# Performance work log

Hardware: AMD Instinct MI355X
Metric: run time of the kernel (lower is better)

Reference implementation:

```python
import jax, jax.numpy as jnp
import numpy as np
import math

P = 7          # patch / kernel size (must be odd for onion-peeling: N = 1+4*m*(m+1) = P*P)
EPS = 1e-6
EPS_W = 0.5

def _ball_dirs():
    u = [np.array([[1.0, 0.0]])]
    s = [np.zeros(1)]
    for k in range(1, P // 2 + 1):
        n = 8 * k
        th = np.linspace(0.0, 2.0 * math.pi * (1.0 - 1.0 / n), n)
        u.append(np.stack([np.cos(th), np.sin(th)], 1))
        s.append(np.full(n, k / (P // 2)))
    return (np.concatenate(u, 0).astype(np.float32), np.concatenate(s).astype(np.float32))

_U, _S = _ball_dirs()  # [N,2], [N], N == P*P == 49

def _forward(x, metric_w, metric_b, proj_w, proj_b):
    B, C, H, W = x.shape
    Hp, Wp = H // P, W // P
    u = jnp.asarray(_U)
    s = jnp.asarray(_S)
    # metric net: strided conv -> 7 params per patch
    params = jax.lax.conv_general_dilated(
        x, metric_w, (P, P), 'VALID',
        dimension_numbers=('NCHW', 'OIHW', 'NCHW')) + metric_b[None, :, None, None]
    v_raw = jnp.moveaxis(params[:, :2], 1, -1)                      # [B,Hp,Wp,2]
    v = v_raw / jnp.maximum(jnp.linalg.norm(v_raw, axis=-1, keepdims=True), 1e-12)
    eig = 2.0 * jax.nn.sigmoid(jnp.moveaxis(params[:, 2:4], 1, -1))  # [B,Hp,Wp,2]
    scale = 0.5 + 1.5 * jax.nn.sigmoid(jnp.moveaxis(params[:, 4:5], 1, -1))
    eig = eig * scale
    vp = jnp.stack([-v[..., 1], v[..., 0]], -1)
    R = jnp.stack([v, vp], -1)                                      # [B,Hp,Wp,2,2] (columns v, v_perp)
    M = R @ (eig[..., None] * jnp.swapaxes(R, -1, -2))              # R diag(eig) R^T
    w = params[:, 5:7]                                              # [B,2,Hp,Wp]
    w = w * (1.0 - EPS_W) * jax.nn.sigmoid(jnp.linalg.norm(w, axis=1, keepdims=True))
    # Finsler-Randers norm F(u) = sqrt(u^T M u + eps) + w.u for all N unit dirs
    quad = jnp.einsum('nj,bhwij,ni->bnhw', u, M, u)                 # [B,N,Hp,Wp]
    drift = jnp.einsum('bihw,ni->bnhw', w, u)
    F_u = jnp.sqrt(quad + EPS) + drift
    y = (u[None, :, :, None, None] / (F_u[:, :, None] + EPS)
         * s[None, :, None, None, None])                            # [B,N,2,Hp,Wp]
    y = y.reshape(B, P, P, 2, Hp, Wp)[:, :, :, ::-1]                # flip last coord pair (x,y)->(y,x)
    gi = jnp.arange(P, dtype=x.dtype) - P // 2
    grid = jnp.stack(jnp.meshgrid(gi, gi, indexing='ij'), -1)       # [P,P,2]
    off = y - grid[None, :, :, :, None, None]                       # [B,P,P,2,Hp,Wp]
    off_y = jnp.transpose(off[:, :, :, 0], (0, 3, 4, 1, 2))         # [B,Hp,Wp,P,P]
    off_x = jnp.transpose(off[:, :, :, 1], (0, 3, 4, 1, 2))
    base_h = (jnp.arange(Hp, dtype=x.dtype) * P)[None, :, None, None, None]
    base_w = (jnp.arange(Wp, dtype=x.dtype) * P)[None, None, :, None, None]
    ki = jnp.arange(P, dtype=x.dtype)
    py = off_y + base_h + ki[None, None, None, :, None]             # sample rows
    px = off_x + base_w + ki[None, None, None, None, :]             # sample cols
    # bilinear sampling with zero padding (torchvision deform_conv2d semantics)
    y0 = jnp.floor(py)
    x0 = jnp.floor(px)
    wy = py - y0
    wx = px - x0

    def gather(yi, xi):
        valid = (yi >= 0) & (yi <= H - 1) & (xi >= 0) & (xi <= W - 1)
        yc = jnp.clip(yi, 0, H - 1).astype(jnp.int32)
        xc = jnp.clip(xi, 0, W - 1).astype(jnp.int32)
        vals = jax.vmap(lambda img, yy, xx: img[:, yy, xx])(x, yc, xc)  # [B,C,Hp,Wp,P,P]
        return vals * valid[:, None].astype(x.dtype)

    sampled = (gather(y0, x0) * ((1 - wy) * (1 - wx))[:, None]
               + gather(y0, x0 + 1) * ((1 - wy) * wx)[:, None]
               + gather(y0 + 1, x0) * (wy * (1 - wx))[:, None]
               + gather(y0 + 1, x0 + 1) * (wy * wx)[:, None])       # [B,C,Hp,Wp,P,P]
    out = jnp.einsum('bchwij,ecij->behw', sampled, proj_w) + proj_b[None, :, None, None]
    return jnp.moveaxis(out.reshape(B, out.shape[1], -1), 1, 2)     # [B, Hp*Wp, E]

def setup_inputs():
    key = jax.random.key(0)
    k0, k1, k2 = jax.random.split(key, 3)
    B, C, H, W, E = 64, 3, 224, 224, 384
    x = jax.random.normal(k0, (B, C, H, W), jnp.float32)
    metric_w = jax.random.normal(k1, (7, C, P, P), jnp.float32) / math.sqrt(C * P * P)
    metric_b = jnp.zeros((7,), jnp.float32)
    proj_w = jax.random.normal(k2, (E, C, P, P), jnp.float32) / (P * math.sqrt(C))
    proj_b = jnp.zeros((E,), jnp.float32)
    return {"x": x, "metric_w": metric_w, "metric_b": metric_b,
            "proj_w": proj_w, "proj_b": proj_b}

def reference(x, metric_w, metric_b, proj_w, proj_b):
    return _forward(x, metric_w, metric_b, proj_w, proj_b)
```

## Files before the change

kernel.cpp:

```cpp
#include <hip/hip_runtime.h>
#include <math.h>

#define PP   7
#define NDIR 49
#define CIN  3
#define KK   147
#define KPAD 160
#define EE   384
#define HH   224
#define WW   224
#define GG   16
#define TB   256
#define SSTR 17
#define NPX  112

typedef __attribute__((ext_vector_type(8))) __bf16 bf16x8;
typedef __attribute__((ext_vector_type(4))) float  f32x4;

__device__ __forceinline__ float sigmoidf_(float v) {
    return 1.0f / (1.0f + expf(-v));
}

__global__ void pack_kernel(const float* __restrict__ x,
                            const float* __restrict__ pw,
                            float* __restrict__ xp,
                            unsigned short* __restrict__ pwB,
                            int npix4) {
    int idx = blockIdx.x * blockDim.x + threadIdx.x;
    if (idx < EE * KPAD) {
        int e = idx / KPAD;
        int k = idx - e * KPAD;
        float v = (k < KK) ? pw[e * KK + k] : 0.0f;
        __bf16 h = (__bf16)v;
        pwB[idx] = *(unsigned short*)&h;
    }
    if (idx < npix4) {
        const int ppi = HH * WW / 4;
        int b = idx / ppi;
        int p = (idx - b * ppi) * 4;
        const float* xb = x + (size_t)b * (CIN * HH * WW) + p;
        f32x4 r0 = *(const f32x4*)(xb);
        f32x4 r1 = *(const f32x4*)(xb + HH * WW);
        f32x4 r2 = *(const f32x4*)(xb + 2 * HH * WW);
        float* op = xp + ((size_t)b * (HH * WW) + p) * 4;
        #pragma unroll
        for (int i = 0; i < 4; ++i) {
            f32x4 v = {r0[i], r1[i], r2[i], 0.0f};
            *(f32x4*)(op + i * 4) = v;
        }
    }
}

template<bool PACKED>
__launch_bounds__(TB, 8)
__global__ void fused_kernel(const float* __restrict__ x,
                             const float* __restrict__ xp,
                             const float* __restrict__ mw,
                             const float* __restrict__ mb,
                             const unsigned short* __restrict__ pwB,
                             const float* __restrict__ pb,
                             float* __restrict__ out) {
    __shared__ float mws[7 * KK];
    __shared__ float dirs[NDIR][3];
    __shared__ float par_s[GG][8];
    __shared__ float der_s[GG][5];
    __shared__ __align__(16) float buf[3136];

    const int t   = threadIdx.x;
    const int blk = blockIdx.x;
    const int b   = blk >> 6;
    const int rem = blk & 63;
    const int hp  = rem >> 1;
    const int wp0 = (rem & 1) * GG;
    const size_t m0 = (size_t)blk * GG;
    const int row0 = hp * PP;
    const int col0 = wp0 * PP;

    for (int i = t; i < 7 * KK; i += TB) mws[i] = mw[i];
    if (t >= 64 && t < 64 + NDIR) {
        int n = t - 64;
        float u0, u1, s;
        if (n == 0)      { u0 = 1.0f; u1 = 0.0f; s = 0.0f; }
        else if (n < 9)  { float th = (float)(n - 1)  * 0.78539816339744831f; u0 = cosf(th); u1 = sinf(th); s = 0.33333334f; }
        else if (n < 25) { float th = (float)(n - 9)  * 0.39269908169872414f; u0 = cosf(th); u1 = sinf(th); s = 0.66666669f; }
        else             { float th = (float)(n - 25) * 0.26179938779914941f; u0 = cosf(th); u1 = sinf(th); s = 1.0f; }
        dirs[n][0] = u0; dirs[n][1] = u1; dirs[n][2] = s;
    }

    if (PACKED) {
        for (int item = t; item < 7 * NPX; item += TB) {
            int i = item / NPX, px = item - i * NPX;
            f32x4 v = *(const f32x4*)(xp + ((size_t)((b * HH + row0 + i) * WW) + col0 + px) * 4);
            *(f32x4*)&buf[item * 4] = v;
        }
    } else {
        for (int item = t; item < CIN * 7 * NPX; item += TB) {
            int c = item / (7 * NPX), r2 = item - c * (7 * NPX);
            int i = r2 / NPX, px = r2 - i * NPX;
            buf[item] = x[(size_t)b * (CIN * HH * WW) + (size_t)c * (HH * WW)
                          + (size_t)(row0 + i) * WW + col0 + px];
        }
    }
    __syncthreads();

    if (t < 112) {
        int prm = t >> 4, g = t & 15;
        float acc = mb[prm];
        const float* wrow = &mws[prm * KK];
        if (PACKED) {
            #pragma unroll 1
            for (int c = 0; c < CIN; ++c) {
                #pragma unroll 1
                for (int i = 0; i < 7; ++i) {
                    const float* bp = &buf[(i * NPX + g * 7) * 4 + c];
                    const float* wr = &wrow[c * 49 + i * 7];
                    #pragma unroll
                    for (int j = 0; j < 7; ++j)
                        acc = fmaf(bp[j * 4], wr[j], acc);
                }
            }
        } else {
            #pragma unroll 1
            for (int c = 0; c < CIN; ++c) {
                #pragma unroll 1
                for (int i = 0; i < 7; ++i) {
                    const float* bp = &buf[(c * 7 + i) * NPX + g * 7];
                    const float* wr = &wrow[c * 49 + i * 7];
                    #pragma unroll
                    for (int j = 0; j < 7; ++j)
                        acc = fmaf(bp[j], wr[j], acc);
                }
            }
        }
        par_s[g][prm] = acc;
    }
    __syncthreads();

    if (t < GG) {
        float a0 = par_s[t][0], a1 = par_s[t][1], a2 = par_s[t][2], a3 = par_s[t][3];
        float a4 = par_s[t][4], a5 = par_s[t][5], a6 = par_s[t][6];
        float nrm = sqrtf(a0 * a0 + a1 * a1);
        float inv = 1.0f / fmaxf(nrm, 1e-12f);
        float v0 = a0 * inv, v1 = a1 * inv;
        float e0 = 2.0f * sigmoidf_(a2);
        float e1 = 2.0f * sigmoidf_(a3);
        float sc = 0.5f + 1.5f * sigmoidf_(a4);
        e0 *= sc; e1 *= sc;
        float wn  = sqrtf(a5 * a5 + a6 * a6);
        float wsc = 0.5f * sigmoidf_(wn);
        der_s[t][0] = e0 * v0 * v0 + e1 * v1 * v1;
        der_s[t][1] = (e0 - e1) * v0 * v1;
        der_s[t][2] = e0 * v1 * v1 + e1 * v0 * v0;
        der_s[t][3] = a5 * wsc;
        der_s[t][4] = a6 * wsc;
    }
    __syncthreads();

    const float* xb = x + (size_t)b * (CIN * HH * WW);
    const size_t pbase = (size_t)b * (HH * WW);
    for (int item = t; item < GG * NDIR; item += TB) {
        int g = item / NDIR;
        int n = item - g * NDIR;
        float u0 = dirs[n][0], u1 = dirs[n][1], s = dirs[n][2];
        float M00 = der_s[g][0], M01 = der_s[g][1], M11 = der_s[g][2];
        float w0 = der_s[g][3], w1 = der_s[g][4];
        float quad  = u0 * u0 * M00 + 2.0f * u0 * u1 * M01 + u1 * u1 * M11;
        float drift = w0 * u0 + w1 * u1;
        float F = sqrtf(quad + 1e-6f) + drift;
        float r = s / (F + 1e-6f);
        float py = (float)(row0 + 3) + u1 * r;
        float px = (float)(col0 + g * PP + 3) + u0 * r;
        float y0f = floorf(py), x0f = floorf(px);
        float y1f = y0f + 1.0f, x1f = x0f + 1.0f;
        float wy = py - y0f, wx = px - x0f;
        bool vy0 = (y0f >= 0.0f) && (y0f <= (float)(HH - 1));
        bool vy1 = (y1f >= 0.0f) && (y1f <= (float)(HH - 1));
        bool vx0 = (x0f >= 0.0f) && (x0f <= (float)(WW - 1));
        bool vx1 = (x1f >= 0.0f) && (x1f <= (float)(WW - 1));
        int iy0 = (int)fminf(fmaxf(y0f, 0.0f), (float)(HH - 1));
        int iy1 = (int)fminf(fmaxf(y1f, 0.0f), (float)(HH - 1));
        int ix0 = (int)fminf(fmaxf(x0f, 0.0f), (float)(WW - 1));
        int ix1 = (int)fminf(fmaxf(x1f, 0.0f), (float)(WW - 1));
        float w00 = (1.0f - wy) * (1.0f - wx);
        float w01 = (1.0f - wy) * wx;
        float w10 = wy * (1.0f - wx);
        float w11 = wy * wx;
        if (PACKED) {
            float c00 = w00 * ((vy0 && vx0) ? 1.0f : 0.0f);
            float c01 = w01 * ((vy0 && vx1) ? 1.0f : 0.0f);
            float c10 = w10 * ((vy1 && vx0) ? 1.0f : 0.0f);
            float c11 = w11 * ((vy1 && vx1) ? 1.0f : 0.0f);
            f32x4 q00 = *(const f32x4*)(xp + (pbase + (size_t)(iy0 * WW + ix0)) * 4);
            f32x4 q01 = *(const f32x4*)(xp + (pbase + (size_t)(iy0 * WW + ix1)) * 4);
            f32x4 q10 = *(const f32x4*)(xp + (pbase + (size_t)(iy1 * WW + ix0)) * 4);
            f32x4 q11 = *(const f32x4*)(xp + (pbase + (size_t)(iy1 * WW + ix1)) * 4);
            #pragma unroll
            for (int c = 0; c < CIN; ++c) {
                buf[(c * NDIR + n) * SSTR + g] =
                    q00[c] * c00 + q01[c] * c01 + q10[c] * c10 + q11[c] * c11;
            }
        } else {
            #pragma unroll
            for (int c = 0; c < CIN; ++c) {
                const float* xc = xb + c * (HH * WW);
                float v00 = (vy0 && vx0) ? xc[iy0 * WW + ix0] : 0.0f;
                float v01 = (vy0 && vx1) ? xc[iy0 * WW + ix1] : 0.0f;
                float v10 = (vy1 && vx0) ? xc[iy1 * WW + ix0] : 0.0f;
                float v11 = (vy1 && vx1) ? xc[iy1 * WW + ix1] : 0.0f;
                buf[(c * NDIR + n) * SSTR + g] =
                    v00 * w00 + v01 * w01 + v10 * w10 + v11 * w11;
            }
        }
    }
    __syncthreads();

    const int lane = t & 63;
    const int wv   = t >> 6;
    const int nrow = lane & 15;
    const int hi   = lane >> 4;

    bf16x8 afr[5];
    #pragma unroll
    for (int ks = 0; ks < 5; ++ks) {
        #pragma unroll
        for (int j = 0; j < 8; ++j) {
            int k = ks * 32 + hi * 8 + j;
            float v = (k < KK) ? buf[k * SSTR + nrow] : 0.0f;
            afr[ks][j] = (__bf16)v;
        }
    }

    #pragma unroll
    for (int q = 0; q < 6; ++q) {
        int tile = wv * 6 + q;
        int e    = tile * 16 + nrow;
        const unsigned short* brow = pwB + (size_t)e * KPAD + hi * 8;
        f32x4 acc = {0.0f, 0.0f, 0.0f, 0.0f};
        #pragma unroll
        for (int ks = 0; ks < 5; ++ks) {
            bf16x8 bfr = *(const bf16x8*)&brow[ks * 32];
            acc = __builtin_amdgcn_mfma_f32_16x16x32_bf16(afr[ks], bfr, acc, 0, 0, 0);
        }
        float bias = pb[e];
        #pragma unroll
        for (int r = 0; r < 4; ++r) {
            out[(m0 + hi * 4 + r) * EE + e] = acc[r] + bias;
        }
    }
}

extern "C" void kernel_launch(void* const* d_in, const int* in_sizes, int n_in,
                              void* d_out, int out_size, void* d_ws, size_t ws_size,
                              hipStream_t stream) {
    const float* x  = (const float*)d_in[0];
    const float* mw = (const float*)d_in[1];
    const float* mb = (const float*)d_in[2];
    const float* pw = (const float*)d_in[3];
    const float* pb = (const float*)d_in[4];
    float* out = (float*)d_out;

    unsigned short* pwB = (unsigned short*)d_ws;
    float* xp = (float*)((char*)d_ws + (size_t)(1 << 17));

    const int B = in_sizes[0] / (CIN * HH * WW);
    const int npix = B * HH * WW;
    const int npix4 = npix / 4;
    const size_t need = (size_t)(1 << 17) + (size_t)npix * 4 * sizeof(float);
    const bool packed = ws_size >= need;

    if (packed) {
        int grid = (npix4 > EE * KPAD ? npix4 : EE * KPAD);
        pack_kernel<<<(grid + 255) / 256, 256, 0, stream>>>(x, pw, xp, pwB, npix4);
        fused_kernel<true><<<B * 64, TB, 0, stream>>>(x, xp, mw, mb, pwB, pb, out);
    } else {
        pack_kernel<<<(EE * KPAD + 255) / 256, 256, 0, stream>>>(x, pw, xp, pwB, 0);
        fused_kernel<false><<<B * 64, TB, 0, stream>>>(x, xp, mw, mb, pwB, pb, out);
    }
}
```

Baseline: 200.1 us.

## Batch bilinear gather loads and transpose MFMA operands for vectorized output stores

Refactors the sampling geometry into a helper and, on the packed path, manually unrolls the gather so two items issue all eight 16-byte loads before any use, with a scheduling barrier to expose memory-level parallelism. Swaps the MFMA operand order so each lane owns four consecutive embedding columns of one token, allowing float4 bias loads and float4 output stores instead of strided scalar stores. Lowers the launch-bounds occupancy hint from 8 to 6 to give the extra in-flight loads register room, at the cost of fewer resident waves.

```diff
diff --git a/kernel.cpp b/kernel.cpp
--- a/kernel.cpp
+++ b/kernel.cpp
@@ -51,8 +51,53 @@
     }
 }
 
+struct GInfo {
+    int g, n;
+    int o00, o01, o10, o11;
+    float c00, c01, c10, c11;
+};
+
+__device__ __forceinline__ GInfo geom_(int item, int row0, int col0,
+                                       const float dirs[NDIR][3],
+                                       const float der[GG][5]) {
+    GInfo r;
+    r.g = item / NDIR;
+    r.n = item - r.g * NDIR;
+    float u0 = dirs[r.n][0], u1 = dirs[r.n][1], s = dirs[r.n][2];
+    float M00 = der[r.g][0], M01 = der[r.g][1], M11 = der[r.g][2];
+    float w0 = der[r.g][3], w1 = der[r.g][4];
+    float quad  = u0 * u0 * M00 + 2.0f * u0 * u1 * M01 + u1 * u1 * M11;
+    float drift = w0 * u0 + w1 * u1;
+    float F = sqrtf(quad + 1e-6f) + drift;
+    float rr = s / (F + 1e-6f);
+    float py = (float)(row0 + 3) + u1 * rr;
+    float px = (float)(col0 + r.g * PP + 3) + u0 * rr;
+    float y0f = floorf(py), x0f = floorf(px);
+    float y1f = y0f + 1.0f, x1f = x0f + 1.0f;
+    float wy = py - y0f, wx = px - x0f;
+    r.c00 = (1.0f - wy) * (1.0f - wx);
+    r.c01 = (1.0f - wy) * wx;
+    r.c10 = wy * (1.0f - wx);
+    r.c11 = wy * wx;
+    bool vy0 = (y0f >= 0.0f) && (y0f <= (float)(HH - 1));
+    bool vy1 = (y1f >= 0.0f) && (y1f <= (float)(HH - 1));
+    bool vx0 = (x0f >= 0.0f) && (x0f <= (float)(WW - 1));
+    bool vx1 = (x1f >= 0.0f) && (x1f <= (float)(WW - 1));
+    r.c00 *= (vy0 && vx0) ? 1.0f : 0.0f;
+    r.c01 *= (vy0 && vx1) ? 1.0f : 0.0f;
+    r.c10 *= (vy1 && vx0) ? 1.0f : 0.0f;
+    r.c11 *= (vy1 && vx1) ? 1.0f : 0.0f;
+    int iy0 = (int)fminf(fmaxf(y0f, 0.0f), (float)(HH - 1));
+    int iy1 = (int)fminf(fmaxf(y1f, 0.0f), (float)(HH - 1));
+    int ix0 = (int)fminf(fmaxf(x0f, 0.0f), (float)(WW - 1));
+    int ix1 = (int)fminf(fmaxf(x1f, 0.0f), (float)(WW - 1));
+    r.o00 = iy0 * WW + ix0; r.o01 = iy0 * WW + ix1;
+    r.o10 = iy1 * WW + ix0; r.o11 = iy1 * WW + ix1;
+    return r;
+}
+
 template<bool PACKED>
-__launch_bounds__(TB, 8)
+__launch_bounds__(TB, 6)
 __global__ void fused_kernel(const float* __restrict__ x,
                              const float* __restrict__ xp,
                              const float* __restrict__ mw,
@@ -87,10 +132,11 @@
         dirs[n][0] = u0; dirs[n][1] = u1; dirs[n][2] = s;
     }
 
+    const size_t pbase = (size_t)b * (HH * WW);
     if (PACKED) {
         for (int item = t; item < 7 * NPX; item += TB) {
             int i = item / NPX, px = item - i * NPX;
-            f32x4 v = *(const f32x4*)(xp + ((size_t)((b * HH + row0 + i) * WW) + col0 + px) * 4);
+            f32x4 v = *(const f32x4*)(xp + (pbase + (size_t)(row0 + i) * WW + col0 + px) * 4);
             *(f32x4*)&buf[item * 4] = v;
         }
     } else {
@@ -156,59 +202,61 @@
     }
     __syncthreads();
 
-    const float* xb = x + (size_t)b * (CIN * HH * WW);
-    const size_t pbase = (size_t)b * (HH * WW);
-    for (int item = t; item < GG * NDIR; item += TB) {
-        int g = item / NDIR;
-        int n = item - g * NDIR;
-        float u0 = dirs[n][0], u1 = dirs[n][1], s = dirs[n][2];
-        float M00 = der_s[g][0], M01 = der_s[g][1], M11 = der_s[g][2];
-        float w0 = der_s[g][3], w1 = der_s[g][4];
-        float quad  = u0 * u0 * M00 + 2.0f * u0 * u1 * M01 + u1 * u1 * M11;
-        float drift = w0 * u0 + w1 * u1;
-        float F = sqrtf(quad + 1e-6f) + drift;
-        float r = s / (F + 1e-6f);
-        float py = (float)(row0 + 3) + u1 * r;
-        float px = (float)(col0 + g * PP + 3) + u0 * r;
-        float y0f = floorf(py), x0f = floorf(px);
-        float y1f = y0f + 1.0f, x1f = x0f + 1.0f;
-        float wy = py - y0f, wx = px - x0f;
-        bool vy0 = (y0f >= 0.0f) && (y0f <= (float)(HH - 1));
-        bool vy1 = (y1f >= 0.0f) && (y1f <= (float)(HH - 1));
-        bool vx0 = (x0f >= 0.0f) && (x0f <= (float)(WW - 1));
-        bool vx1 = (x1f >= 0.0f) && (x1f <= (float)(WW - 1));
-        int iy0 = (int)fminf(fmaxf(y0f, 0.0f), (float)(HH - 1));
-        int iy1 = (int)fminf(fmaxf(y1f, 0.0f), (float)(HH - 1));
-        int ix0 = (int)fminf(fmaxf(x0f, 0.0f), (float)(WW - 1));
-        int ix1 = (int)fminf(fmaxf(x1f, 0.0f), (float)(WW - 1));
-        float w00 = (1.0f - wy) * (1.0f - wx);
-        float w01 = (1.0f - wy) * wx;
-        float w10 = wy * (1.0f - wx);
-        float w11 = wy * wx;
-        if (PACKED) {
-            float c00 = w00 * ((vy0 && vx0) ? 1.0f : 0.0f);
-            float c01 = w01 * ((vy0 && vx1) ? 1.0f : 0.0f);
-            float c10 = w10 * ((vy1 && vx0) ? 1.0f : 0.0f);
-            float c11 = w11 * ((vy1 && vx1) ? 1.0f : 0.0f);
-            f32x4 q00 = *(const f32x4*)(xp + (pbase + (size_t)(iy0 * WW + ix0)) * 4);
-            f32x4 q01 = *(const f32x4*)(xp + (pbase + (size_t)(iy0 * WW + ix1)) * 4);
-            f32x4 q10 = *(const f32x4*)(xp + (pbase + (size_t)(iy1 * WW + ix0)) * 4);
-            f32x4 q11 = *(const f32x4*)(xp + (pbase + (size_t)(iy1 * WW + ix1)) * 4);
-            #pragma unroll
-            for (int c = 0; c < CIN; ++c) {
-                buf[(c * NDIR + n) * SSTR + g] =
-                    q00[c] * c00 + q01[c] * c01 + q10[c] * c10 + q11[c] * c11;
-            }
-        } else {
+    if (PACKED) {
+        const float* base = xp + pbase * 4;
+        {
+            GInfo A = geom_(t,      row0, col0, dirs, der_s);
+            GInfo B = geom_(t + TB, row0, col0, dirs, der_s);
+            f32x4 qa0 = *(const f32x4*)(base + (size_t)A.o00 * 4);
+            f32x4 qa1 = *(const f32x4*)(base + (size_t)A.o01 * 4);
+            f32x4 qa2 = *(const f32x4*)(base + (size_t)A.o10 * 4);
+            f32x4 qa3 = *(const f32x4*)(base + (size_t)A.o11 * 4);
+            f32x4 qb0 = *(const f32x4*)(base + (size_t)B.o00 * 4);
+            f32x4 qb1 = *(const f32x4*)(base + (size_t)B.o01 * 4);
+            f32x4 qb2 = *(const f32x4*)(base + (size_t)B.o10 * 4);
+            f32x4 qb3 = *(const f32x4*)(base + (size_t)B.o11 * 4);
+            __builtin_amdgcn_sched_barrier(0);
+            #pragma unroll
+            for (int c = 0; c < CIN; ++c)
+                buf[(c * NDIR + A.n) * SSTR + A.g] =
+                    qa0[c] * A.c00 + qa1[c] * A.c01 + qa2[c] * A.c10 + qa3[c] * A.c11;
+            #pragma unroll
+            for (int c = 0; c < CIN; ++c)
+                buf[(c * NDIR + B.n) * SSTR + B.g] =
+                    qb0[c] * B.c00 + qb1[c] * B.c01 + qb2[c] * B.c10 + qb3[c] * B.c11;
+        }
+        {
+            GInfo C = geom_(t + 2 * TB, row0, col0, dirs, der_s);
+            f32x4 q0 = *(const f32x4*)(base + (size_t)C.o00 * 4);
+            f32x4 q1 = *(const f32x4*)(base + (size_t)C.o01 * 4);
+            f32x4 q2 = *(const f32x4*)(base + (size_t)C.o10 * 4);
+            f32x4 q3 = *(const f32x4*)(base + (size_t)C.o11 * 4);
+            #pragma unroll
+            for (int c = 0; c < CIN; ++c)
+                buf[(c * NDIR + C.n) * SSTR + C.g] =
+                    q0[c] * C.c00 + q1[c] * C.c01 + q2[c] * C.c10 + q3[c] * C.c11;
+        }
+        if (t < GG * NDIR - 3 * TB) {
+            GInfo D = geom_(t + 3 * TB, row0, col0, dirs, der_s);
+            f32x4 q0 = *(const f32x4*)(base + (size_t)D.o00 * 4);
+            f32x4 q1 = *(const f32x4*)(base + (size_t)D.o01 * 4);
+            f32x4 q2 = *(const f32x4*)(base + (size_t)D.o10 * 4);
+            f32x4 q3 = *(const f32x4*)(base + (size_t)D.o11 * 4);
+            #pragma unroll
+            for (int c = 0; c < CIN; ++c)
+                buf[(c * NDIR + D.n) * SSTR + D.g] =
+                    q0[c] * D.c00 + q1[c] * D.c01 + q2[c] * D.c10 + q3[c] * D.c11;
+        }
+    } else {
+        const float* xb = x + (size_t)b * (CIN * HH * WW);
+        for (int item = t; item < GG * NDIR; item += TB) {
+            GInfo A = geom_(item, row0, col0, dirs, der_s);
             #pragma unroll
             for (int c = 0; c < CIN; ++c) {
                 const float* xc = xb + c * (HH * WW);
-                float v00 = (vy0 && vx0) ? xc[iy0 * WW + ix0] : 0.0f;
-                float v01 = (vy0 && vx1) ? xc[iy0 * WW + ix1] : 0.0f;
-                float v10 = (vy1 && vx0) ? xc[iy1 * WW + ix0] : 0.0f;
-                float v11 = (vy1 && vx1) ? xc[iy1 * WW + ix1] : 0.0f;
-                buf[(c * NDIR + n) * SSTR + g] =
-                    v00 * w00 + v01 * w01 + v10 * w10 + v11 * w11;
+                buf[(c * NDIR + A.n) * SSTR + A.g] =
+                    xc[A.o00] * A.c00 + xc[A.o01] * A.c01 +
+                    xc[A.o10] * A.c10 + xc[A.o11] * A.c11;
             }
         }
     }
@@ -219,33 +267,33 @@
     const int nrow = lane & 15;
     const int hi   = lane >> 4;
 
-    bf16x8 afr[5];
+    bf16x8 sfr[5];
     #pragma unroll
     for (int ks = 0; ks < 5; ++ks) {
         #pragma unroll
         for (int j = 0; j < 8; ++j) {
             int k = ks * 32 + hi * 8 + j;
             float v = (k < KK) ? buf[k * SSTR + nrow] : 0.0f;
-            afr[ks][j] = (__bf16)v;
-        }
-    }
-
+            sfr[ks][j] = (__bf16)v;
+        }
+    }
+
+    float* orow = out + (m0 + nrow) * EE;
     #pragma unroll
     for (int q = 0; q < 6; ++q) {
         int tile = wv * 6 + q;
-        int e    = tile * 16 + nrow;
-        const unsigned short* brow = pwB + (size_t)e * KPAD + hi * 8;
+        int erow = tile * 16 + nrow;
+        const unsigned short* arow = pwB + (size_t)erow * KPAD + hi * 8;
         f32x4 acc = {0.0f, 0.0f, 0.0f, 0.0f};
         #pragma unroll
         for (int ks = 0; ks < 5; ++ks) {
-            bf16x8 bfr = *(const bf16x8*)&brow[ks * 32];
-            acc = __builtin_amdgcn_mfma_f32_16x16x32_bf16(afr[ks], bfr, acc, 0, 0, 0);
-        }
-        float bias = pb[e];
-        #pragma unroll
-        for (int r = 0; r < 4; ++r) {
-            out[(m0 + hi * 4 + r) * EE + e] = acc[r] + bias;
-        }
+            bf16x8 afr = *(const bf16x8*)&arow[ks * 32];
+            acc = __builtin_amdgcn_mfma_f32_16x16x32_bf16(afr, sfr[ks], acc, 0, 0, 0);
+        }
+        int e0 = tile * 16 + hi * 4;
+        f32x4 b4 = *(const f32x4*)&pb[e0];
+        f32x4 o = acc + b4;
+        *(f32x4*)&orow[e0] = o;
     }
 }
 
```

After: 210.5 us. +5.2%, slower.
